# Performance work log

Hardware: AMD Instinct MI355X
Metric: run time of the kernel (lower is better)

## Reference

```python
import jax, jax.numpy as jnp
import numpy as np
import math

B, C, H, W = 8, 384, 14, 14
HEADS = 12
HC = C // HEADS
STRIDE = 2
K = 3
FACTOR = 2.0
rH = -(-H // STRIDE)
rW = -(-W // STRIDE)
N = H * W
S = rH * rW
KK = K * K
OFFSET_MAT = np.array([[0, -1], [-1, -1], [-1, 0], [-1, 1], [0, 1], [1, 1], [1, 0], [1, -1], [0, 0]], dtype=np.float32)


def bilinear_sample(img, coords):
    """img (Hi,Wi,C); coords (...,2) normalized (y,x) in [-1,1].
    Matches F.grid_sample(mode='bilinear', align_corners=True, padding_mode='zeros')."""
    Hi, Wi = img.shape[0], img.shape[1]
    py = (coords[..., 0] + 1.0) * 0.5 * (Hi - 1)
    px = (coords[..., 1] + 1.0) * 0.5 * (Wi - 1)
    y0 = jnp.floor(py)
    x0 = jnp.floor(px)
    wy1 = py - y0
    wx1 = px - x0

    def corner(yf, xf, wgt):
        valid = (yf >= 0) & (yf <= Hi - 1) & (xf >= 0) & (xf <= Wi - 1)
        yi = jnp.clip(yf, 0, Hi - 1).astype(jnp.int32)
        xi = jnp.clip(xf, 0, Wi - 1).astype(jnp.int32)
        return img[yi, xi] * (wgt * valid)[..., None]

    return (corner(y0, x0, (1 - wy1) * (1 - wx1)) + corner(y0, x0 + 1, (1 - wy1) * wx1)
            + corner(y0 + 1, x0, wy1 * (1 - wx1)) + corner(y0 + 1, x0 + 1, wy1 * wx1))


def _forward(x, Wq, bq, Wk, bk, Wv, bv, Wo1, bo1, Wdw, bdw, ln_g, ln_b, Wo2, Wco, posembed, Wp, bp):
    dt = x.dtype
    xh = jnp.transpose(x, (0, 2, 3, 1))                       # B,H,W,C
    q = jnp.einsum('bhwc,oc->bhwo', xh, Wq) + bq              # q_conv (1x1)

    # ---- offset network: 1x1 conv -> GELU -> 3x3 dw stride conv -> LN -> GELU -> 1x1 ----
    t = jax.nn.gelu(jnp.einsum('bhwc,oc->bhwo', q, Wo1) + bo1, approximate=False)
    ker = jnp.transpose(Wdw, (2, 3, 1, 0))                    # (3,3,1,C) for HWIO depthwise
    t = jax.lax.conv_general_dilated(t, ker, (STRIDE, STRIDE), ((1, 1), (1, 1)),
                                     dimension_numbers=('NHWC', 'HWIO', 'NHWC'),
                                     feature_group_count=C) + bdw  # B,rH,rW,C
    mu = t.mean(-1, keepdims=True)
    var = ((t - mu) ** 2).mean(-1, keepdims=True)
    t = (t - mu) / jnp.sqrt(var + 1e-5) * ln_g + ln_b
    t = jax.nn.gelu(t, approximate=False)
    off = jnp.einsum('bhwc,oc->bhwo', t, Wo2)                 # B,rH,rW,2*N ; channel = (g,h,w)
    off = off.reshape(B, rH, rW, 2, N)
    off = jnp.transpose(off, (0, 3, 4, 1, 2))                 # B,2,N,rH,rW
    ranges = jnp.array([1.0 / H, 1.0 / W], dtype=dt)
    off = jnp.tanh(off) * ranges[None, :, None, None, None] * FACTOR
    off = jnp.transpose(off, (0, 2, 3, 4, 1))                 # B,N,rH,rW,2 (y,x)

    # ---- strided reference grid + deformable bilinear gather from x ----
    gy = jnp.arange(0, H, STRIDE, dtype=dt) / (H - 1) * 2 - 1
    gx = jnp.arange(0, W, STRIDE, dtype=dt) / (W - 1) * 2 - 1
    ref = jnp.stack(jnp.meshgrid(gy, gx, indexing='ij'), -1)  # rH,rW,2
    dpos = off + ref
    sampled = jax.vmap(bilinear_sample)(xh, dpos).reshape(B, N, S, C)

    # ---- k x k center points with learned offsets ----
    cy = jnp.arange(H, dtype=dt)
    cx = jnp.arange(W, dtype=dt)
    center = jnp.stack(jnp.meshgrid(cy, cx, indexing='ij'), -1).reshape(N, 1, 2)
    offmat = jnp.asarray(OFFSET_MAT, dtype=dt)
    cpt = center + offmat[None]                               # N,KK,2
    cpt_norm = jnp.stack([jnp.clip(cpt[..., 0], 0, H) / (H - 1) * 2 - 1,
                          jnp.clip(cpt[..., 1], 0, W) / (W - 1) * 2 - 1], -1).reshape(N, K, K, 2)
    q_tok = q.reshape(B, N, C)
    co = jnp.tanh(jnp.einsum('bnc,oc->bno', q_tok, Wco).reshape(B, N, K, K, 2)) * ranges
    cgrid = co + cpt_norm[None]
    csampled = jax.vmap(bilinear_sample)(xh, cgrid).reshape(B, N, KK, C)

    feats = jnp.concatenate([sampled, csampled], axis=2)      # B,N,S+KK,C
    k = (jnp.einsum('bnsc,oc->bnso', feats, Wk) + bk).reshape(B, N, S + KK, HEADS, HC)
    v = (jnp.einsum('bnsc,oc->bnso', feats, Wv) + bv).reshape(B, N, S + KK, HEADS, HC)
    qh = q_tok.reshape(B, N, HEADS, HC)
    attn = jnp.einsum('bnhd,bnshd->bhns', qh, k)              # qk_scale=None -> no scaling

    # ---- dynamic relative position bias (grid_sample into rel-pos table) ----
    a = jnp.arange(0, H, STRIDE, dtype=dt)
    bcol = jnp.arange(0, W, dtype=dt)
    ref_pos = a[None, :] - bcol[:, None]                      # (W, rH)
    ref_pos_x = jnp.tile(ref_pos, (H, rH))                    # (N, S)
    ref_pos_y = jnp.repeat(jnp.repeat(ref_pos, W, axis=0), rW, axis=1)
    rpp = jnp.stack([ref_pos_y / (H - 1), ref_pos_x / (W - 1)], -1)  # N,S,2
    rel = rpp.reshape(N, rH, rW, 2)[None] - off               # B,N,rH,rW,2
    table = jnp.transpose(posembed, (1, 2, 0))                # (2H-1, 2W-1, heads)
    d_rel = bilinear_sample(table, rel).reshape(B, N, S, HEADS)
    cpt_raw = jnp.broadcast_to(center, (N, KK, 2)).reshape(N, K, K, 2)
    crel = co - cpt_raw[None]
    d_crel = bilinear_sample(table, crel).reshape(B, N, KK, HEADS)
    bias = jnp.concatenate([d_rel, d_crel], axis=2)           # B,N,S+KK,heads
    attn = attn + jnp.transpose(bias, (0, 3, 1, 2))
    attn = jax.nn.softmax(attn, axis=-1)

    out = jnp.einsum('bhns,bnshd->bnhd', attn, v).reshape(B, N, C)
    out = jnp.einsum('bnc,oc->bno', out, Wp) + bp             # proj (1x1)
    return jnp.transpose(out.reshape(B, H, W, C), (0, 3, 1, 2))


def setup_inputs() -> dict:
    key = jax.random.key(0)
    ks = jax.random.split(key, 20)
    def w(k, shape, s=0.05):
        return jax.random.normal(k, shape, dtype=jnp.float32) * s
    return {
        'x': jax.random.normal(ks[0], (B, C, H, W), dtype=jnp.float32),
        'Wq': w(ks[1], (C, C)), 'bq': w(ks[2], (C,)),
        'Wk': w(ks[3], (C, C)), 'bk': w(ks[4], (C,)),
        'Wv': w(ks[5], (C, C)), 'bv': w(ks[6], (C,)),
        'Wo1': w(ks[7], (C, C)), 'bo1': w(ks[8], (C,)),
        'Wdw': w(ks[9], (C, 1, 3, 3), 0.2), 'bdw': w(ks[10], (C,)),
        'ln_g': jnp.ones((C,), jnp.float32), 'ln_b': jnp.zeros((C,), jnp.float32),
        'Wo2': w(ks[11], (2 * N, C)),
        'Wco': w(ks[12], (2 * K * K, C)),
        'posembed': w(ks[13], (HEADS, 2 * H - 1, 2 * W - 1), 0.02),
        'Wp': w(ks[14], (C, C)), 'bp': w(ks[15], (C,)),
    }


def reference(x, Wq, bq, Wk, bk, Wv, bv, Wo1, bo1, Wdw, bdw, ln_g, ln_b, Wo2, Wco, posembed, Wp, bp):
    return _forward(x, Wq, bq, Wk, bk, Wv, bv, Wo1, bo1, Wdw, bdw, ln_g, ln_b, Wo2, Wco, posembed, Wp, bp)
```

## Files before the change

kernel.cpp:

```cpp
#include <hip/hip_runtime.h>
#include <hip/hip_bf16.h>
#include <math.h>

#define BB 8
#define CC 384
#define HH 14
#define WW 14
#define NHEADS 12
#define RH 7
#define RW 7
#define NN 196
#define SS 49
#define KKK 9
#define SK 58
#define TH 27
#define NTOK 1568
#define WSZ 147456
#define WO2SZ 150528

typedef float    f4 __attribute__((ext_vector_type(4)));
typedef _Float16 h8 __attribute__((ext_vector_type(8)));
typedef _Float16 h4 __attribute__((ext_vector_type(4)));

__device__ __forceinline__ float geluf(float x){ return 0.5f*x*(1.0f+erff(x*0.7071067811865475f)); }
__device__ __forceinline__ f4 mfma16h(h8 a, h8 b, f4 c){
  return __builtin_amdgcn_mfma_f32_16x16x32_f16(a, b, c, 0, 0, 0);
}

__constant__ float c_offm[9][2] = {{0,-1},{-1,-1},{-1,0},{-1,1},{0,1},{1,1},{1,0},{1,-1},{0,0}};

__global__ void __launch_bounds__(256) k_pre(const float* __restrict__ x,
    _Float16* __restrict__ xhh,
    const float* __restrict__ Wq, const float* __restrict__ Wk, const float* __restrict__ Wo1,
    const float* __restrict__ Wp, const float* __restrict__ Wv, const float* __restrict__ Wo2,
    _Float16* __restrict__ Wh){
  __shared__ float tile[48*203];
  int bid = blockIdx.x;
  int t = threadIdx.x;
  if (bid < 64){
    int b = bid >> 3, c0 = (bid & 7)*48;
    for (int i = t; i < 48*49; i += 256){
      int row = i / 49, seg = i % 49;
      f4 v = *(const f4*)(x + ((size_t)(b*CC + c0 + row))*NN + seg*4);
      #pragma unroll
      for (int j = 0; j < 4; ++j) tile[row*203 + seg*4 + j] = v[j];
    }
    __syncthreads();
    for (int i = t; i < 196*12; i += 256){
      int n = i / 12, seg = i % 12;
      h4 vh;
      #pragma unroll
      for (int j = 0; j < 4; ++j) vh[j] = (_Float16)tile[(seg*4 + j)*203 + n];
      *(h4*)(xhh + ((size_t)(b*NN + n))*CC + c0 + seg*4) = vh;
    }
  } else if (bid < 424){
    int bid2 = bid - 64;
    int mat = bid2 / 72;
    int e0 = (bid2 % 72)*2048 + t*8;
    const float* src = mat==0?Wq: mat==1?Wk: mat==2?Wo1: mat==3?Wp: Wv;
    f4 v0 = *(const f4*)(src + e0);
    f4 v1 = *(const f4*)(src + e0 + 4);
    h8 hi;
    #pragma unroll
    for (int j = 0; j < 4; ++j){ hi[j] = (_Float16)v0[j]; hi[4+j] = (_Float16)v1[j]; }
    *(h8*)(Wh + (size_t)mat*WSZ + e0) = hi;
  } else {
    int e0 = (bid - 424)*2048 + t*8;
    if (e0 < WO2SZ){
      f4 v0 = *(const f4*)(Wo2 + e0);
      f4 v1 = *(const f4*)(Wo2 + e0 + 4);
      h8 hi;
      #pragma unroll
      for (int j = 0; j < 4; ++j){ hi[j] = (_Float16)v0[j]; hi[4+j] = (_Float16)v1[j]; }
      *(h8*)(Wh + (size_t)5*WSZ + e0) = hi;
    }
  }
}

__device__ __forceinline__ void gemm_fp16_body(
    const _Float16* __restrict__ Ahg, const _Float16* __restrict__ Bhg,
    int arow, int brow, _Float16* sbuf, int t, f4 acc[4]){
  _Float16* Ah = sbuf; _Float16* Bh = sbuf + 2560;
  int w = t>>6, lane = t&63, col = lane&15, quad = lane>>4;
  int r = t>>2, cg = t&3;
  const _Float16* Arh = Ahg + (size_t)arow*384 + cg*8;
  const _Float16* Brh = Bhg + (size_t)brow*384 + cg*8;
  h8 ah = *(const h8*)(Arh);
  h8 bh = *(const h8*)(Brh);
  for (int k0 = 0; k0 < 384; k0 += 32){
    __syncthreads();
    *(h8*)(Ah + r*40 + cg*8) = ah;
    *(h8*)(Bh + r*40 + cg*8) = bh;
    __syncthreads();
    if (k0 < 352){
      ah = *(const h8*)(Arh + k0 + 32);
      bh = *(const h8*)(Brh + k0 + 32);
    }
    h8 afh = *(const h8*)(Ah + (w*16+col)*40 + quad*8);
    #pragma unroll
    for (int nt = 0; nt < 4; ++nt){
      h8 bfh = *(const h8*)(Bh + (nt*16+col)*40 + quad*8);
      acc[nt] = mfma16h(afh, bfh, acc[nt]);
    }
  }
}

__global__ void __launch_bounds__(256) k_qkv(
    const _Float16* __restrict__ xhh,
    const _Float16* __restrict__ Wh,
    const float* __restrict__ bq,
    float* __restrict__ qf, _Float16* __restrict__ qfh,
    _Float16* __restrict__ K2h, _Float16* __restrict__ VprojT){
  __shared__ __align__(16) _Float16 sbuf[5120];
  int t = threadIdx.x;
  int w = t>>6, lane = t&63, col = lane&15, quad = lane>>4;
  int bid = blockIdx.x;

  if (bid < 300){
    int isK = (bid >= 150) ? 1 : 0;
    int r2 = isK ? bid - 150 : bid;
    const _Float16* Bh = Wh + (size_t)(isK ? 1 : 0)*WSZ;
    int m0 = (r2/6)*64, n0 = (r2%6)*64;
    int r = t>>2;
    int arow = min(m0 + r, NTOK-1);
    int brow = n0 + r;
    f4 acc[4] = {{0,0,0,0},{0,0,0,0},{0,0,0,0},{0,0,0,0}};
    gemm_fp16_body(xhh, Bh, arow, brow, sbuf, t, acc);
    #pragma unroll
    for (int nt = 0; nt < 4; ++nt){
      #pragma unroll
      for (int rr = 0; rr < 4; ++rr){
        int m = m0 + w*16 + quad*4 + rr;
        int o = n0 + nt*16 + col;
        if (m >= NTOK) continue;
        if (isK){
          K2h[(size_t)m*384 + o] = (_Float16)acc[nt][rr];
        } else {
          float v = acc[nt][rr] + bq[o];
          qf[(size_t)m*384 + o] = v;
          qfh[(size_t)m*384 + o] = (_Float16)v;
        }
      }
    }
  } else {
    int idx = bid - 300;
    int mo = idx % 6;
    int ny = (idx / 6) % 4;
    int b  = idx / 24;
    int m0 = mo*64, n0 = ny*64;
    int orow = m0 + w*16 + col;
    const _Float16* wvh = Wh + (size_t)4*WSZ + (size_t)orow*384;
    f4 acc[4] = {{0,0,0,0},{0,0,0,0},{0,0,0,0},{0,0,0,0}};
    for (int kt = 0; kt < 12; ++kt){
      h8 ah = *(const h8*)(wvh + kt*32 + quad*8);
      #pragma unroll
      for (int nt = 0; nt < 4; ++nt){
        int i = min(n0 + nt*16 + col, 195);
        h8 b8 = *(const h8*)(xhh + ((size_t)(b*196 + i))*384 + kt*32 + quad*8);
        acc[nt] = mfma16h(ah, b8, acc[nt]);
      }
    }
    #pragma unroll
    for (int nt = 0; nt < 4; ++nt){
      #pragma unroll
      for (int rr = 0; rr < 4; ++rr){
        int o = m0 + w*16 + quad*4 + rr;
        int i = n0 + nt*16 + col;
        if (i < 224)
          VprojT[((size_t)(b*384 + o))*224 + i] = (i < 196) ? (_Float16)acc[nt][rr] : (_Float16)0.f;
      }
    }
  }
}

__global__ void __launch_bounds__(256) k_mid(
    const _Float16* __restrict__ qfh,
    const _Float16* __restrict__ Wh,
    const float* __restrict__ bo1, float* __restrict__ t1,
    const _Float16* __restrict__ K2h, _Float16* __restrict__ G16){
  __shared__ __align__(16) _Float16 sbuf[5120];
  int t = threadIdx.x;
  int w = t>>6, lane = t&63, col = lane&15, quad = lane>>4;
  int bid = blockIdx.x;
  if (bid < 150){
    const _Float16* Bh = Wh + (size_t)2*WSZ;
    int m0 = (bid/6)*64, n0 = (bid%6)*64;
    int r = t>>2;
    int arow = min(m0 + r, NTOK-1);
    int brow = n0 + r;
    f4 acc[4] = {{0,0,0,0},{0,0,0,0},{0,0,0,0},{0,0,0,0}};
    gemm_fp16_body(qfh, Bh, arow, brow, sbuf, t, acc);
    #pragma unroll
    for (int nt = 0; nt < 4; ++nt){
      #pragma unroll
      for (int rr = 0; rr < 4; ++rr){
        int m = m0 + w*16 + quad*4 + rr;
        int o = n0 + nt*16 + col;
        if (m >= NTOK) continue;
        t1[(size_t)m*384 + o] = geluf(acc[nt][rr] + bo1[o]);
      }
    }
  } else {
    int idx = bid - 150;
    int m0 = (idx & 3)*64;
    int bh = idx >> 2; int b = bh / 12, h = bh - b*12;
    const _Float16* qr = qfh + ((size_t)(b*196 + min(m0 + w*16 + col, 195)))*384 + h*32;
    h8 a8 = *(const h8*)(qr + quad*8);
    f4 acc[13];
    #pragma unroll
    for (int nt = 0; nt < 13; ++nt){
      int i = min(nt*16 + col, 195);
      h8 b8 = *(const h8*)(K2h + ((size_t)(b*196 + i))*384 + h*32 + quad*8);
      f4 z = {0.f,0.f,0.f,0.f};
      acc[nt] = mfma16h(a8, b8, z);
    }
    #pragma unroll
    for (int nt = 0; nt < 13; ++nt){
      #pragma unroll
      for (int r = 0; r < 4; ++r){
        int m = m0 + w*16 + quad*4 + r;
        int i = nt*16 + col;
        if (m < 196 && i < 196)
          G16[((size_t)(b*196 + m))*2352 + h*196 + i] = (_Float16)acc[nt][r];
      }
    }
  }
}

__global__ void __launch_bounds__(384) k_dwln(const float* __restrict__ t1,
      const float* __restrict__ Wdw, const float* __restrict__ bdw,
      const float* __restrict__ lng, const float* __restrict__ lnb,
      _Float16* __restrict__ t2h){
  int blk = blockIdx.x;
  int ow = blk % RW; int oh = (blk / RW) % RH; int b = blk / (RH*RW);
  int c = threadIdx.x;
  float acc = bdw[c];
  #pragma unroll
  for (int kh = 0; kh < 3; ++kh){
    int ih = oh*2 - 1 + kh;
    if (ih < 0 || ih >= HH) continue;
    #pragma unroll
    for (int kw = 0; kw < 3; ++kw){
      int iw = ow*2 - 1 + kw;
      if (iw < 0 || iw >= WW) continue;
      acc += t1[((b*HH + ih)*WW + iw)*CC + c] * Wdw[c*9 + kh*3 + kw];
    }
  }
  __shared__ float red[6];
  __shared__ float s_mu, s_rv;
  float v = acc;
  #pragma unroll
  for (int o = 32; o > 0; o >>= 1) v += __shfl_down(v, o);
  int wid = c >> 6, lane = c & 63;
  if (lane == 0) red[wid] = v;
  __syncthreads();
  if (c == 0){ float s = 0.f; for (int i = 0; i < 6; ++i) s += red[i]; s_mu = s / CC; }
  __syncthreads();
  float mu = s_mu;
  float d = acc - mu;
  v = d*d;
  #pragma unroll
  for (int o = 32; o > 0; o >>= 1) v += __shfl_down(v, o);
  if (lane == 0) red[wid] = v;
  __syncthreads();
  if (c == 0){ float s = 0.f; for (int i = 0; i < 6; ++i) s += red[i]; s_rv = rsqrtf(s / CC + 1e-5f); }
  __syncthreads();
  float val = geluf(d * s_rv * lng[c] + lnb[c]);
  t2h[blk*CC + c] = (_Float16)val;
}

__global__ void __launch_bounds__(256) k_off(
    const _Float16* __restrict__ t2h,
    const _Float16* __restrict__ Wh,
    float* __restrict__ offp){
  __shared__ __align__(16) _Float16 sbuf[5120];
  int t = threadIdx.x;
  int w = t>>6, lane = t&63, col = lane&15, quad = lane>>4;
  int bid = blockIdx.x;
  int m0 = (bid/7)*64, n0 = (bid%7)*64;
  int r = t>>2;
  int arow = min(m0 + r, 391);
  int brow = min(n0 + r, 391);
  const _Float16* Bh = Wh + (size_t)5*WSZ;
  f4 acc[4] = {{0,0,0,0},{0,0,0,0},{0,0,0,0},{0,0,0,0}};
  gemm_fp16_body(t2h, Bh, arow, brow, sbuf, t, acc);
  #pragma unroll
  for (int nt = 0; nt < 4; ++nt){
    #pragma unroll
    for (int rr = 0; rr < 4; ++rr){
      int row = m0 + w*16 + quad*4 + rr;
      int o = n0 + nt*16 + col;
      if (row < 392 && o < 392){
        int g = o / NN, nn = o % NN;
        int b = row / SS, s = row % SS;
        float rng = (g == 0) ? (1.0f/HH) : (1.0f/WW);
        offp[((b*NN + nn)*SS + s)*2 + g] = tanhf(acc[nt][rr]) * rng * 2.0f;
      }
    }
  }
}

__global__ void __launch_bounds__(256, 7) k_fused(
    const float* __restrict__ qf, const float* __restrict__ off,
    const _Float16* __restrict__ G16,
    const float* __restrict__ bk, const float* __restrict__ Wco, const float* __restrict__ pos,
    _Float16* __restrict__ agg16){
  __shared__ __align__(16) _Float16 Gs[2352];
  __shared__ __align__(16) float agg[12*228];
  __shared__ float scoreS[696];
  __shared__ float offl[98];
  __shared__ float colb[18];
  __shared__ float qbv[12];
  __shared__ uint2 tapv[232];
  float* qrow = agg;

  int blk = blockIdx.x;
  int n = blk % NN, b = blk / NN;
  int iy = n / WW, ix = n % WW;
  int t = threadIdx.x;

  {
    const h8* g8 = (const h8*)(G16 + (size_t)blk*2352);
    h8* gs8 = (h8*)Gs;
    for (int i = t; i < 294; i += 256) gs8[i] = g8[i];
  }
  {
    const f4* q4 = (const f4*)(qf + (size_t)blk*384);
    f4* qr4 = (f4*)qrow;
    for (int i = t; i < 96; i += 256) qr4[i] = q4[i];
  }
  for (int i = t; i < 98; i += 256) offl[i] = off[(size_t)blk*98 + i];
  __syncthreads();

  if (t < 144){
    int o = t >> 3, l = t & 7;
    const float* wr = Wco + o*384 + l*48;
    const float* qr = qrow + l*48;
    f4 a4 = {0.f,0.f,0.f,0.f};
    #pragma unroll
    for (int c = 0; c < 48; c += 4) a4 += (*(const f4*)(qr + c)) * (*(const f4*)(wr + c));
    float acc = a4[0]+a4[1]+a4[2]+a4[3];
    acc += __shfl_xor(acc, 1); acc += __shfl_xor(acc, 2); acc += __shfl_xor(acc, 4);
    if (l == 0){
      int g = o & 1;
      float range = (g == 0) ? (1.0f/HH) : (1.0f/WW);
      colb[o] = tanhf(acc) * range;
    }
  }
  if (t >= 160){
    int o = t - 160;
    int h = o >> 3, l = o & 7;
    float acc = 0.f;
    for (int d = l; d < 32; d += 8) acc += qrow[h*32 + d] * bk[h*32 + d];
    acc += __shfl_xor(acc, 1); acc += __shfl_xor(acc, 2); acc += __shfl_xor(acc, 4);
    if (l == 0 && h < 12) qbv[h] = acc;
  }
  __syncthreads();

  if (t < SK){
    float cy, cx;
    if (t < SS){
      int sy = t / RW, sx = t % RW;
      cy = offl[t*2+0] + ((2.0f*sy)/13.0f*2.0f - 1.0f);
      cx = offl[t*2+1] + ((2.0f*sx)/13.0f*2.0f - 1.0f);
    } else {
      int kk = t - SS;
      float cyr = fminf(fmaxf((float)iy + c_offm[kk][0], 0.f), (float)HH);
      float cxr = fminf(fmaxf((float)ix + c_offm[kk][1], 0.f), (float)WW);
      cy = colb[kk*2+0] + (cyr/13.0f*2.0f - 1.0f);
      cx = colb[kk*2+1] + (cxr/13.0f*2.0f - 1.0f);
    }
    float py = (cy + 1.0f)*0.5f*13.0f;
    float px = (cx + 1.0f)*0.5f*13.0f;
    float y0 = floorf(py), x0 = floorf(px);
    float wy1 = py - y0, wx1 = px - x0;
    #pragma unroll
    for (int k4 = 0; k4 < 4; ++k4){
      float yf = y0 + (k4 >> 1), xf = x0 + (k4 & 1);
      bool valid = (yf >= 0.f) && (yf <= 13.f) && (xf >= 0.f) && (xf <= 13.f);
      int yi = (int)fminf(fmaxf(yf, 0.f), 13.f);
      int xi = (int)fminf(fmaxf(xf, 0.f), 13.f);
      float wgt = ((k4 >> 1) ? wy1 : (1.f - wy1)) * ((k4 & 1) ? wx1 : (1.f - wx1));
      tapv[t*4 + k4] = make_uint2(__float_as_uint(valid ? wgt : 0.f),
                                  (unsigned)(yi*WW + xi));
    }
  }
  __syncthreads();
  for (int i = t; i < 12*228; i += 256) agg[i] = 0.f;

  if (t < 232){
    int s = t >> 2, grp = t & 3;
    float ry, rx;
    if (s < SS){
      int sy = s / RW, sx = s % RW;
      ry = (2.0f*sy - iy)/13.0f - offl[s*2+0];
      rx = (2.0f*sx - ix)/13.0f - offl[s*2+1];
    } else {
      int kk = s - SS;
      ry = colb[kk*2+0] - (float)iy;
      rx = colb[kk*2+1] - (float)ix;
    }
    float py = (ry + 1.0f)*0.5f*26.0f;
    float px = (rx + 1.0f)*0.5f*26.0f;
    float y0 = floorf(py), x0 = floorf(px);
    float wy1 = py - y0, wx1 = px - x0;
    int pidx[4]; float pw[4];
    #pragma unroll
    for (int k4 = 0; k4 < 4; ++k4){
      float yf = y0 + (k4 >> 1), xf = x0 + (k4 & 1);
      bool valid = (yf >= 0.f) && (yf <= 26.f) && (xf >= 0.f) && (xf <= 26.f);
      int yi = (int)fminf(fmaxf(yf, 0.f), 26.f);
      int xi = (int)fminf(fmaxf(xf, 0.f), 26.f);
      pidx[k4] = yi*TH + xi;
      float wgt = ((k4 >> 1) ? wy1 : (1.f - wy1)) * ((k4 & 1) ? wx1 : (1.f - wx1));
      pw[k4] = valid ? wgt : 0.f;
    }
    uint2 tp0 = tapv[s*4+0], tp1 = tapv[s*4+1], tp2 = tapv[s*4+2], tp3 = tapv[s*4+3];
    float tw0 = __uint_as_float(tp0.x), tw1 = __uint_as_float(tp1.x);
    float tw2 = __uint_as_float(tp2.x), tw3 = __uint_as_float(tp3.x);
    #pragma unroll
    for (int hh = 0; hh < 3; ++hh){
      int h = grp*3 + hh;
      const float* pt = pos + h*729;
      float val = qbv[h];
      val += pt[pidx[0]]*pw[0];
      val += pt[pidx[1]]*pw[1];
      val += pt[pidx[2]]*pw[2];
      val += pt[pidx[3]]*pw[3];
      const _Float16* gh = Gs + h*196;
      val += tw0*(float)gh[(int)tp0.y];
      val += tw1*(float)gh[(int)tp1.y];
      val += tw2*(float)gh[(int)tp2.y];
      val += tw3*(float)gh[(int)tp3.y];
      scoreS[h*58 + s] = val;
    }
  }
  __syncthreads();

  if (t < 192){
    int h = t >> 4, l = t & 15;
    float v[4];
    #pragma unroll
    for (int k = 0; k < 4; ++k){ int s = l + 16*k; v[k] = (s < SK) ? scoreS[h*58 + s] : -1e30f; }
    float mx = fmaxf(fmaxf(v[0], v[1]), fmaxf(v[2], v[3]));
    mx = fmaxf(mx, __shfl_xor(mx, 1)); mx = fmaxf(mx, __shfl_xor(mx, 2));
    mx = fmaxf(mx, __shfl_xor(mx, 4)); mx = fmaxf(mx, __shfl_xor(mx, 8));
    float e[4], sum = 0.f;
    #pragma unroll
    for (int k = 0; k < 4; ++k){ int s = l + 16*k; e[k] = (s < SK) ? expf(v[k] - mx) : 0.f; sum += e[k]; }
    sum += __shfl_xor(sum, 1); sum += __shfl_xor(sum, 2);
    sum += __shfl_xor(sum, 4); sum += __shfl_xor(sum, 8);
    float inv = 1.0f / sum;
    #pragma unroll
    for (int k = 0; k < 4; ++k){
      int s = l + 16*k;
      if (s < SK) scoreS[h*58 + s] = e[k]*inv;
    }
  }
  __syncthreads();

  if (t < 232){
    uint2 tp = tapv[t];
    float wv = __uint_as_float(tp.x);
    if (wv != 0.f){
      int s = t >> 2, cell = (int)tp.y;
      float* ag = agg + cell;
      #pragma unroll
      for (int h = 0; h < 12; ++h)
        atomicAdd(ag + h*228, scoreS[h*58 + s]*wv);
    }
  }
  __syncthreads();

  {
    _Float16* ar = agg16 + (size_t)blk*2688;
    for (int i = t; i < 336; i += 256){
      int d = i*8;
      int h = d / 224, j = d - h*224;
      const float* src = agg + h*228 + j;
      f4 a = *(const f4*)src;
      f4 c = *(const f4*)(src + 4);
      h8 o;
      #pragma unroll
      for (int k = 0; k < 4; ++k){ o[k] = (_Float16)a[k]; o[4+k] = (_Float16)c[k]; }
      *(h8*)(ar + d) = o;
    }
  }
}

__global__ void __launch_bounds__(256) k_av(const _Float16* __restrict__ agg16,
                                            const _Float16* __restrict__ VprojT,
                                            const float* __restrict__ bv,
                                            _Float16* __restrict__ otokh){
  int t = threadIdx.x;
  int w = t>>6, lane = t&63, col = lane&15, quad = lane>>4;
  int m0 = blockIdx.x*64;
  int bh = blockIdx.y; int b = bh / 12, h = bh - b*12;
  const _Float16* ar = agg16 + ((size_t)(b*196 + min(m0 + w*16 + col, 195)))*2688 + h*224;
  f4 acc[2] = {{0,0,0,0},{0,0,0,0}};
  for (int kt = 0; kt < 7; ++kt){
    h8 a8 = *(const h8*)(ar + kt*32 + quad*8);
    #pragma unroll
    for (int nt = 0; nt < 2; ++nt){
      int o = h*32 + nt*16 + col;
      h8 b8 = *(const h8*)(VprojT + ((size_t)(b*384 + o))*224 + kt*32 + quad*8);
      acc[nt] = mfma16h(a8, b8, acc[nt]);
    }
  }
  #pragma unroll
  for (int nt = 0; nt < 2; ++nt){
    #pragma unroll
    for (int rr = 0; rr < 4; ++rr){
      int m = m0 + w*16 + quad*4 + rr;
      if (m < 196){
        int o = h*32 + nt*16 + col;
        float v = acc[nt][rr] + bv[o];
        otokh[((size_t)(b*196 + m))*384 + o] = (_Float16)v;
      }
    }
  }
}

__global__ void __launch_bounds__(256) k_proj(
    const _Float16* __restrict__ otokh,
    const _Float16* __restrict__ Wh,
    const float* __restrict__ bias, float* __restrict__ out){
  __shared__ __align__(16) _Float16 sbuf[5120];
  __shared__ float tile[16*65];
  int t = threadIdx.x;
  int w = t>>6, lane = t&63, col = lane&15, quad = lane>>4;
  int m0 = blockIdx.x*64, n0 = blockIdx.y*64;
  int r = t>>2;
  int arow = min(m0 + r, NTOK-1);
  int brow = n0 + r;
  const _Float16* Bh = Wh + (size_t)3*WSZ;
  f4 acc[4] = {{0,0,0,0},{0,0,0,0},{0,0,0,0},{0,0,0,0}};
  gemm_fp16_body(otokh, Bh, arow, brow, sbuf, t, acc);
  float* tl = (float*)sbuf;
  __syncthreads();
  #pragma unroll
  for (int nt = 0; nt < 4; ++nt)
    #pragma unroll
    for (int rr = 0; rr < 4; ++rr)
      tile[(w*16 + quad*4 + rr)%16*65 + nt*16 + col] = 0.f;
  __syncthreads();
  #pragma unroll
  for (int pass = 0; pass < 4; ++pass){
    __syncthreads();
    if (w == pass){
      #pragma unroll
      for (int nt = 0; nt < 4; ++nt)
        #pragma unroll
        for (int rr = 0; rr < 4; ++rr)
          tile[(quad*4 + rr)*65 + nt*16 + col] = acc[nt][rr];
    }
    __syncthreads();
    for (int i = t; i < 256; i += 256){
      int o_l = i >> 2, ms = i & 3;
      int m = m0 + pass*16 + ms*4;
      if (m >= NTOK) continue;
      int bb = m / NN, nnn = m % NN;
      int o = n0 + o_l;
      float bo = bias[o];
      f4 v = { tile[(ms*4+0)*65 + o_l] + bo, tile[(ms*4+1)*65 + o_l] + bo,
               tile[(ms*4+2)*65 + o_l] + bo, tile[(ms*4+3)*65 + o_l] + bo };
      *(f4*)(out + ((size_t)bb*384 + o)*NN + nnn) = v;
    }
  }
}

extern "C" void kernel_launch(void* const* d_in, const int* in_sizes, int n_in,
                              void* d_out, int out_size, void* d_ws, size_t ws_size,
                              hipStream_t stream){
  const float* x    = (const float*)d_in[0];
  const float* Wq   = (const float*)d_in[1];
  const float* bq   = (const float*)d_in[2];
  const float* Wk   = (const float*)d_in[3];
  const float* bk   = (const float*)d_in[4];
  const float* Wv   = (const float*)d_in[5];
  const float* bv   = (const float*)d_in[6];
  const float* Wo1  = (const float*)d_in[7];
  const float* bo1  = (const float*)d_in[8];
  const float* Wdw  = (const float*)d_in[9];
  const float* bdw  = (const float*)d_in[10];
  const float* ln_g = (const float*)d_in[11];
  const float* ln_b = (const float*)d_in[12];
  const float* Wo2  = (const float*)d_in[13];
  const float* Wco  = (const float*)d_in[14];
  const float* pos  = (const float*)d_in[15];
  const float* Wp   = (const float*)d_in[16];
  const float* bp   = (const float*)d_in[17];
  float* out = (float*)d_out;

  float* ws   = (float*)d_ws;
  float* qf   = ws;
  float* t1   = qf   + 602112;
  float* offp = t1   + 602112;
  _Float16* xhh    = (_Float16*)(offp + 153664);
  _Float16* qfh    = xhh    + 602112;
  _Float16* t2h    = qfh    + 602112;
  _Float16* K2h    = t2h    + 150528;
  _Float16* VprojT = K2h    + 602112;
  _Float16* otokh  = VprojT + 688128;
  _Float16* Wh     = otokh  + 602112;
  _Float16* G16    = Wh     + 5*WSZ + WO2SZ;
  _Float16* agg16  = G16    + 3687936;

  k_pre<<<498, 256, 0, stream>>>(x, xhh, Wq, Wk, Wo1, Wp, Wv, Wo2, Wh);
  k_qkv<<<492, 256, 0, stream>>>(xhh, Wh, bq, qf, qfh, K2h, VprojT);
  k_mid<<<534, 256, 0, stream>>>(qfh, Wh, bo1, t1, K2h, G16);
  k_dwln<<<392, 384, 0, stream>>>(t1, Wdw, bdw, ln_g, ln_b, t2h);
  k_off<<<49, 256, 0, stream>>>(t2h, Wh, offp);
  k_fused<<<1568, 256, 0, stream>>>(qf, offp, G16, bk, Wco, pos, agg16);
  k_av<<<dim3(4,96), 256, 0, stream>>>(agg16, VprojT, bv, otokh);
  k_proj<<<dim3(25,6), 256, 0, stream>>>(otokh, Wh, bp, out);
}
```

Before: 181.6 us.

## Map each token to one wavefront in fused attention kernel, drop block barriers

The fused deformable-attention kernel now handles two tokens per 128-thread block, one wavefront per token, each with its own shared-memory slice. All block-wide __syncthreads are replaced by wave-level barriers with LDS waitcnt fences, and the per-stage work is reorganised into loops over lanes. This removes block-synchronisation overhead and idle threads in the many small stages, but it gives less parallelism per token, since one wave now does all 12 heads' score computation. It also removes a redundant tile-zeroing pass and two barriers in the projection kernel.

```diff
diff --git a/kernel.cpp b/kernel.cpp
--- a/kernel.cpp
+++ b/kernel.cpp
@@ -17,6 +17,7 @@
 #define NTOK 1568
 #define WSZ 147456
 #define WO2SZ 150528
+#define TOKSZ 16096
 
 typedef float    f4 __attribute__((ext_vector_type(4)));
 typedef _Float16 h8 __attribute__((ext_vector_type(8)));
@@ -26,6 +27,9 @@
 __device__ __forceinline__ f4 mfma16h(h8 a, h8 b, f4 c){
   return __builtin_amdgcn_mfma_f32_16x16x32_f16(a, b, c, 0, 0, 0);
 }
+#define WAVE_FENCE() do{ __builtin_amdgcn_wave_barrier(); \
+  asm volatile("s_waitcnt lgkmcnt(0)" ::: "memory"); \
+  __builtin_amdgcn_wave_barrier(); }while(0)
 
 __constant__ float c_offm[9][2] = {{0,-1},{-1,-1},{-1,0},{-1,1},{0,1},{1,1},{1,0},{1,-1},{0,0}};
 
@@ -300,71 +304,79 @@
   }
 }
 
-__global__ void __launch_bounds__(256, 7) k_fused(
+__global__ void __launch_bounds__(128) k_fused(
     const float* __restrict__ qf, const float* __restrict__ off,
     const _Float16* __restrict__ G16,
     const float* __restrict__ bk, const float* __restrict__ Wco, const float* __restrict__ pos,
     _Float16* __restrict__ agg16){
-  __shared__ __align__(16) _Float16 Gs[2352];
-  __shared__ __align__(16) float agg[12*228];
-  __shared__ float scoreS[696];
-  __shared__ float offl[98];
-  __shared__ float colb[18];
-  __shared__ float qbv[12];
-  __shared__ uint2 tapv[232];
-  float* qrow = agg;
-
-  int blk = blockIdx.x;
+  __shared__ __align__(16) char smem[2*TOKSZ];
+  int tid = threadIdx.x;
+  int tk = tid >> 6, lane = tid & 63;
+  int blk = blockIdx.x*2 + tk;
+  char* base = smem + tk*TOKSZ;
+  float*    scoreS = (float*)base;
+  uint2*    tapv   = (uint2*)(base + 2784);
+  float*    colb   = (float*)(base + 4640);
+  float*    qbv    = (float*)(base + 4712);
+  float*    offl   = (float*)(base + 4760);
+  float*    qrow   = (float*)(base + 5152);
+  _Float16* Gs     = (_Float16*)(base + 5152 + 1536);
+  float*    agg    = (float*)(base + 5152);
+
   int n = blk % NN, b = blk / NN;
   int iy = n / WW, ix = n % WW;
-  int t = threadIdx.x;
 
   {
     const h8* g8 = (const h8*)(G16 + (size_t)blk*2352);
     h8* gs8 = (h8*)Gs;
-    for (int i = t; i < 294; i += 256) gs8[i] = g8[i];
+    for (int i = lane; i < 294; i += 64) gs8[i] = g8[i];
   }
   {
     const f4* q4 = (const f4*)(qf + (size_t)blk*384);
     f4* qr4 = (f4*)qrow;
-    for (int i = t; i < 96; i += 256) qr4[i] = q4[i];
-  }
-  for (int i = t; i < 98; i += 256) offl[i] = off[(size_t)blk*98 + i];
-  __syncthreads();
-
-  if (t < 144){
-    int o = t >> 3, l = t & 7;
-    const float* wr = Wco + o*384 + l*48;
-    const float* qr = qrow + l*48;
-    f4 a4 = {0.f,0.f,0.f,0.f};
-    #pragma unroll
-    for (int c = 0; c < 48; c += 4) a4 += (*(const f4*)(qr + c)) * (*(const f4*)(wr + c));
-    float acc = a4[0]+a4[1]+a4[2]+a4[3];
-    acc += __shfl_xor(acc, 1); acc += __shfl_xor(acc, 2); acc += __shfl_xor(acc, 4);
-    if (l == 0){
-      int g = o & 1;
-      float range = (g == 0) ? (1.0f/HH) : (1.0f/WW);
-      colb[o] = tanhf(acc) * range;
-    }
-  }
-  if (t >= 160){
-    int o = t - 160;
-    int h = o >> 3, l = o & 7;
-    float acc = 0.f;
-    for (int d = l; d < 32; d += 8) acc += qrow[h*32 + d] * bk[h*32 + d];
-    acc += __shfl_xor(acc, 1); acc += __shfl_xor(acc, 2); acc += __shfl_xor(acc, 4);
-    if (l == 0 && h < 12) qbv[h] = acc;
-  }
-  __syncthreads();
-
-  if (t < SK){
+    for (int i = lane; i < 96; i += 64) qr4[i] = q4[i];
+  }
+  for (int i = lane; i < 98; i += 64) offl[i] = off[(size_t)blk*98 + i];
+  WAVE_FENCE();
+
+  #pragma unroll
+  for (int p = 0; p < 3; ++p){
+    int o = p*8 + (lane>>3), l = lane&7;
+    if (o < 18){
+      const float* wr = Wco + o*384 + l*48;
+      const float* qr = qrow + l*48;
+      f4 a4 = {0.f,0.f,0.f,0.f};
+      #pragma unroll
+      for (int c = 0; c < 48; c += 4) a4 += (*(const f4*)(qr + c)) * (*(const f4*)(wr + c));
+      float acc = a4[0]+a4[1]+a4[2]+a4[3];
+      acc += __shfl_xor(acc, 1); acc += __shfl_xor(acc, 2); acc += __shfl_xor(acc, 4);
+      if (l == 0){
+        int g = o & 1;
+        float range = (g == 0) ? (1.0f/HH) : (1.0f/WW);
+        colb[o] = tanhf(acc) * range;
+      }
+    }
+  }
+  #pragma unroll
+  for (int p = 0; p < 2; ++p){
+    int h = p*8 + (lane>>3), l = lane&7;
+    if (h < 12){
+      float acc = 0.f;
+      for (int d = l; d < 32; d += 8) acc += qrow[h*32 + d] * bk[h*32 + d];
+      acc += __shfl_xor(acc, 1); acc += __shfl_xor(acc, 2); acc += __shfl_xor(acc, 4);
+      if (l == 0) qbv[h] = acc;
+    }
+  }
+  WAVE_FENCE();
+
+  if (lane < SK){
     float cy, cx;
-    if (t < SS){
-      int sy = t / RW, sx = t % RW;
-      cy = offl[t*2+0] + ((2.0f*sy)/13.0f*2.0f - 1.0f);
-      cx = offl[t*2+1] + ((2.0f*sx)/13.0f*2.0f - 1.0f);
+    if (lane < SS){
+      int sy = lane / RW, sx = lane % RW;
+      cy = offl[lane*2+0] + ((2.0f*sy)/13.0f*2.0f - 1.0f);
+      cx = offl[lane*2+1] + ((2.0f*sx)/13.0f*2.0f - 1.0f);
     } else {
-      int kk = t - SS;
+      int kk = lane - SS;
       float cyr = fminf(fmaxf((float)iy + c_offm[kk][0], 0.f), (float)HH);
       float cxr = fminf(fmaxf((float)ix + c_offm[kk][1], 0.f), (float)WW);
       cy = colb[kk*2+0] + (cyr/13.0f*2.0f - 1.0f);
@@ -381,15 +393,14 @@
       int yi = (int)fminf(fmaxf(yf, 0.f), 13.f);
       int xi = (int)fminf(fmaxf(xf, 0.f), 13.f);
       float wgt = ((k4 >> 1) ? wy1 : (1.f - wy1)) * ((k4 & 1) ? wx1 : (1.f - wx1));
-      tapv[t*4 + k4] = make_uint2(__float_as_uint(valid ? wgt : 0.f),
-                                  (unsigned)(yi*WW + xi));
-    }
-  }
-  __syncthreads();
-  for (int i = t; i < 12*228; i += 256) agg[i] = 0.f;
-
-  if (t < 232){
-    int s = t >> 2, grp = t & 3;
+      tapv[lane*4 + k4] = make_uint2(__float_as_uint(valid ? wgt : 0.f),
+                                     (unsigned)(yi*WW + xi));
+    }
+  }
+  WAVE_FENCE();
+
+  if (lane < SK){
+    int s = lane;
     float ry, rx;
     if (s < SS){
       int sy = s / RW, sx = s % RW;
@@ -419,8 +430,7 @@
     float tw0 = __uint_as_float(tp0.x), tw1 = __uint_as_float(tp1.x);
     float tw2 = __uint_as_float(tp2.x), tw3 = __uint_as_float(tp3.x);
     #pragma unroll
-    for (int hh = 0; hh < 3; ++hh){
-      int h = grp*3 + hh;
+    for (int h = 0; h < NHEADS; ++h){
       const float* pt = pos + h*729;
       float val = qbv[h];
       val += pt[pidx[0]]*pw[0];
@@ -435,10 +445,13 @@
       scoreS[h*58 + s] = val;
     }
   }
-  __syncthreads();
-
-  if (t < 192){
-    int h = t >> 4, l = t & 15;
+  WAVE_FENCE();
+
+  for (int i = lane; i < 12*228; i += 64) agg[i] = 0.f;
+
+  #pragma unroll
+  for (int p = 0; p < 3; ++p){
+    int h = p*4 + (lane>>4), l = lane&15;
     float v[4];
     #pragma unroll
     for (int k = 0; k < 4; ++k){ int s = l + 16*k; v[k] = (s < SK) ? scoreS[h*58 + s] : -1e30f; }
@@ -457,24 +470,24 @@
       if (s < SK) scoreS[h*58 + s] = e[k]*inv;
     }
   }
-  __syncthreads();
-
-  if (t < 232){
-    uint2 tp = tapv[t];
+  WAVE_FENCE();
+
+  for (int tap = lane; tap < 232; tap += 64){
+    uint2 tp = tapv[tap];
     float wv = __uint_as_float(tp.x);
     if (wv != 0.f){
-      int s = t >> 2, cell = (int)tp.y;
+      int s = tap >> 2, cell = (int)tp.y;
       float* ag = agg + cell;
       #pragma unroll
       for (int h = 0; h < 12; ++h)
         atomicAdd(ag + h*228, scoreS[h*58 + s]*wv);
     }
   }
-  __syncthreads();
+  WAVE_FENCE();
 
   {
     _Float16* ar = agg16 + (size_t)blk*2688;
-    for (int i = t; i < 336; i += 256){
+    for (int i = lane; i < 336; i += 64){
       int d = i*8;
       int h = d / 224, j = d - h*224;
       const float* src = agg + h*228 + j;
@@ -536,14 +549,6 @@
   const _Float16* Bh = Wh + (size_t)3*WSZ;
   f4 acc[4] = {{0,0,0,0},{0,0,0,0},{0,0,0,0},{0,0,0,0}};
   gemm_fp16_body(otokh, Bh, arow, brow, sbuf, t, acc);
-  float* tl = (float*)sbuf;
-  __syncthreads();
-  #pragma unroll
-  for (int nt = 0; nt < 4; ++nt)
-    #pragma unroll
-    for (int rr = 0; rr < 4; ++rr)
-      tile[(w*16 + quad*4 + rr)%16*65 + nt*16 + col] = 0.f;
-  __syncthreads();
   #pragma unroll
   for (int pass = 0; pass < 4; ++pass){
     __syncthreads();
@@ -611,7 +616,7 @@
   k_mid<<<534, 256, 0, stream>>>(qfh, Wh, bo1, t1, K2h, G16);
   k_dwln<<<392, 384, 0, stream>>>(t1, Wdw, bdw, ln_g, ln_b, t2h);
   k_off<<<49, 256, 0, stream>>>(t2h, Wh, offp);
-  k_fused<<<1568, 256, 0, stream>>>(qf, offp, G16, bk, Wco, pos, agg16);
+  k_fused<<<784, 128, 0, stream>>>(qf, offp, G16, bk, Wco, pos, agg16);
   k_av<<<dim3(4,96), 256, 0, stream>>>(agg16, VprojT, bv, otokh);
   k_proj<<<dim3(25,6), 256, 0, stream>>>(otokh, Wh, bp, out);
 }
```

After: 190.9 us. 1.05x slower.
